# Kernel optimization log

Measured on AMD Instinct MI355X. Metric: run time of the kernel, lower is better.

Reference implementation:

```python
import jax, jax.numpy as jnp
import numpy as np

N, C, TX, TY = 32, 256, 1024, 1024


def setup_inputs() -> dict:
    key = jax.random.key(0)
    ks = jax.random.split(key, 9)
    s = 1.0 / np.sqrt(C)
    return {
        "Q": jax.random.normal(ks[0], (N, C, TY), dtype=jnp.float32),
        "K": jax.random.normal(ks[1], (N, C, TX), dtype=jnp.float32),
        "V": jax.random.normal(ks[2], (N, C, TX), dtype=jnp.float32),
        "Wq": jax.random.normal(ks[3], (C, C), dtype=jnp.float32) * s,
        "bq": jax.random.normal(ks[4], (C,), dtype=jnp.float32) * 0.01,
        "Wk": jax.random.normal(ks[5], (C, C), dtype=jnp.float32) * s,
        "bk": jax.random.normal(ks[6], (C,), dtype=jnp.float32) * 0.01,
        "Wv": jax.random.normal(ks[7], (C, C), dtype=jnp.float32) * s,
        "bv": jax.random.normal(ks[8], (C,), dtype=jnp.float32) * 0.01,
    }


def _proj_tanh(W, b, x):
    # 1x1 conv over channels: (C_out, C_in) x (N, C_in, T) -> (N, C_out, T)
    return jnp.tanh(jnp.einsum("oc,nct->not", W, x) + b[None, :, None])


def reference(Q, K, V, Wq, bq, Wk, bk, Wv, bv):
    d_k = Q.shape[1]
    Qp = _proj_tanh(Wq, bq, Q)  # (N, C, Ty)
    Kp = _proj_tanh(Wk, bk, K)  # (N, C, Tx)
    Vp = _proj_tanh(Wv, bv, V)  # (N, C, Tx)
    scores = jnp.einsum("ncs,nct->nst", Kp, Qp) / jnp.sqrt(
        jnp.asarray(d_k, dtype=Q.dtype)
    )  # (N, Tx, Ty)
    A = jax.nn.softmax(scores, axis=1)  # softmax over Tx (dim=1)
    R = jnp.einsum("ncs,nst->nct", Vp, A)  # (N, C, Ty)
    return (R, A)
```

## Files before the change

### kernel.cpp

```cpp
#include <hip/hip_runtime.h>
#include <stdint.h>

#define N_B 32
#define C_D 256
#define T_D 1024

typedef unsigned short u16;
typedef __attribute__((ext_vector_type(8))) short short8;
typedef __attribute__((ext_vector_type(4))) float f32x4;

__device__ __forceinline__ u16 f2bf(float f) {
    unsigned x = __float_as_uint(f);
    return (u16)((x + 0x7fffu + ((x >> 16) & 1u)) >> 16);
}

__device__ __forceinline__ void gld16(const void* g, void* l) {
    __builtin_amdgcn_global_load_lds(
        (const __attribute__((address_space(1))) uint32_t*)g,
        (__attribute__((address_space(3))) uint32_t*)l, 16, 0, 0);
}

__device__ __forceinline__ void comb(float& m, float& l, float m2, float l2) {
    float M = fmaxf(m, m2);
    l = l * __expf(m - M) + l2 * __expf(m2 - M);
    m = M;
}

__global__ __launch_bounds__(256) void conv_w(const float* __restrict__ w0,
                                              const float* __restrict__ w1,
                                              const float* __restrict__ w2,
                                              u16* __restrict__ o0,
                                              u16* __restrict__ o1,
                                              u16* __restrict__ o2) {
    const float* in = blockIdx.y == 0 ? w0 : (blockIdx.y == 1 ? w1 : w2);
    u16* out       = blockIdx.y == 0 ? o0 : (blockIdx.y == 1 ? o1 : o2);
    int i = blockIdx.x * 256 + threadIdx.x;
    out[i] = f2bf(in[i]);
}

template <bool NORM>
__device__ __forceinline__ void stage_tr(const float* src, u16* sm, int tid,
                                         const float* Mv, const float* Rv,
                                         float* adst, bool awr) {
    const int sr2 = tid >> 4;
    const int tt8 = (tid & 15) * 8;
    float4 v0 = *(const float4*)(src);
    float4 v1 = *(const float4*)(src + 4);
    float4 w0 = *(const float4*)(src + T_D);
    float4 w1 = *(const float4*)(src + T_D + 4);
    float a[8] = {v0.x, v0.y, v0.z, v0.w, v1.x, v1.y, v1.z, v1.w};
    float b[8] = {w0.x, w0.y, w0.z, w0.w, w1.x, w1.y, w1.z, w1.w};
    if constexpr (NORM) {
#pragma unroll
        for (int j = 0; j < 8; ++j) {
            a[j] = __expf(a[j] - Mv[j]) * Rv[j];
            b[j] = __expf(b[j] - Mv[j]) * Rv[j];
        }
        if (awr) {
            ((float4*)adst)[0]         = make_float4(a[0], a[1], a[2], a[3]);
            ((float4*)adst)[1]         = make_float4(a[4], a[5], a[6], a[7]);
            ((float4*)(adst + T_D))[0] = make_float4(b[0], b[1], b[2], b[3]);
            ((float4*)(adst + T_D))[1] = make_float4(b[4], b[5], b[6], b[7]);
        }
    }
    const int kk = sr2 * 2;
#pragma unroll
    for (int j = 0; j < 8; ++j) {
        const int t  = tt8 + j;
        const int ks = kk ^ (((t >> 4) & 3) << 3);
        uint32_t pk = (uint32_t)f2bf(a[j]) | ((uint32_t)f2bf(b[j]) << 16);
        *(uint32_t*)(sm + t * 32 + ks) = pk;
    }
}

template <bool TRA, bool TRB, int EPI, bool F32OUT>
__global__ __launch_bounds__(256) void gemm_t(
        const void* __restrict__ Av, const void* __restrict__ Bv,
        const float* __restrict__ bias, void* __restrict__ OutV,
        int Kdim, int ldo, long sA, long sB, long sO, float scale,
        float* __restrict__ Pm, float* __restrict__ Pl)
{
    __shared__ __align__(16) u16 smA[128 * 32];
    __shared__ __align__(16) u16 smB[128 * 32];

    const int nb = blockIdx.z;
    const int n0 = blockIdx.x * 128;
    const int m0 = blockIdx.y * 128;
    const int tid = threadIdx.x;

    const int srow = tid >> 2;
    const int sk8  = (tid & 3) * 8;
    const int sr2  = tid >> 4;
    const int tt8  = (tid & 15) * 8;

    const u16* gA0 = nullptr; const u16* gA1 = nullptr;
    const float* tA = nullptr;
    if constexpr (TRA) {
        tA = (const float*)Av + (size_t)nb * sA + (size_t)(sr2 * 2) * T_D + m0 + tt8;
    } else {
        const u16* Ab = (const u16*)Av + (size_t)nb * sA;
        gA0 = Ab + (size_t)(m0 + srow) * Kdim + sk8;
        gA1 = gA0 + (size_t)64 * Kdim;
    }
    const u16* gB0 = nullptr; const u16* gB1 = nullptr;
    const float* tB = nullptr;
    if constexpr (TRB) {
        tB = (const float*)Bv + (size_t)nb * sB + (size_t)(sr2 * 2) * T_D + n0 + tt8;
    } else {
        const u16* Bb = (const u16*)Bv + (size_t)nb * sB;
        gB0 = Bb + (size_t)(n0 + srow) * Kdim + sk8;
        gB1 = gB0 + (size_t)64 * Kdim;
    }
    u16* lA0 = smA + tid * 8; u16* lA1 = smA + 2048 + tid * 8;
    u16* lB0 = smB + tid * 8; u16* lB1 = smB + 2048 + tid * 8;

    const int lane = tid & 63;
    const int w    = tid >> 6;
    const int wm   = (w >> 1) * 64;
    const int wn   = (w & 1) * 64;
    const int l15  = lane & 15;
    const int quad = lane >> 4;

    f32x4 acc[4][4];
#pragma unroll
    for (int i = 0; i < 4; ++i)
#pragma unroll
        for (int j = 0; j < 4; ++j) acc[i][j] = (f32x4){0.f, 0.f, 0.f, 0.f};

    for (int kb = 0; kb < Kdim; kb += 32) {
        if constexpr (TRA) {
            stage_tr<false>(tA + (size_t)kb * T_D, smA, tid, nullptr, nullptr, nullptr, false);
        } else {
            gld16(gA0 + kb, lA0);
            gld16(gA1 + kb, lA1);
        }
        if constexpr (TRB) {
            stage_tr<false>(tB + (size_t)kb * T_D, smB, tid, nullptr, nullptr, nullptr, false);
        } else {
            gld16(gB0 + kb, lB0);
            gld16(gB1 + kb, lB1);
        }
        __syncthreads();
        short8 af[4], bfr[4];
#pragma unroll
        for (int i = 0; i < 4; ++i) {
            const int ra = wm + i * 16 + l15;
            const int ca = TRA ? ((quad ^ ((ra >> 4) & 3)) * 8) : (quad * 8);
            af[i] = *(const short8*)(smA + ra * 32 + ca);
            const int rb = wn + i * 16 + l15;
            const int cb = TRB ? ((quad ^ ((rb >> 4) & 3)) * 8) : (quad * 8);
            bfr[i] = *(const short8*)(smB + rb * 32 + cb);
        }
#pragma unroll
        for (int mi = 0; mi < 4; ++mi)
#pragma unroll
            for (int ni = 0; ni < 4; ++ni)
                acc[mi][ni] = __builtin_amdgcn_mfma_f32_16x16x32_bf16(
                        af[mi], bfr[ni], acc[mi][ni], 0, 0, 0);
        __syncthreads();
    }

    if constexpr (EPI == 3) {
        float pmv[4] = {-1e30f, -1e30f, -1e30f, -1e30f};
        float plv[4] = {0.f, 0.f, 0.f, 0.f};
#pragma unroll
        for (int mi = 0; mi < 4; ++mi) {
            const int mb = m0 + wm + mi * 16 + quad * 4;
#pragma unroll
            for (int r = 0; r < 4; ++r) {
                const int m = mb + r;
#pragma unroll
                for (int ni = 0; ni < 4; ++ni) {
                    const int nn = n0 + wn + ni * 16 + l15;
                    float v = acc[mi][ni][r] * scale;
                    ((float*)OutV)[(size_t)nb * sO + (size_t)m * ldo + nn] = v;
                    pmv[ni] = fmaxf(pmv[ni], v);
                }
            }
        }
#pragma unroll
        for (int ni = 0; ni < 4; ++ni) {
            float s = 0.f;
#pragma unroll
            for (int mi = 0; mi < 4; ++mi)
#pragma unroll
                for (int r = 0; r < 4; ++r)
                    s += __expf(acc[mi][ni][r] * scale - pmv[ni]);
            plv[ni] = s;
        }
#pragma unroll
        for (int ni = 0; ni < 4; ++ni) {
            float m = pmv[ni], l = plv[ni];
            float m2 = __shfl_xor(m, 16), l2 = __shfl_xor(l, 16);
            comb(m, l, m2, l2);
            m2 = __shfl_xor(m, 32); l2 = __shfl_xor(l, 32);
            comb(m, l, m2, l2);
            pmv[ni] = m; plv[ni] = l;
        }
        __shared__ float red_m[4][64];
        __shared__ float red_l[4][64];
        if (quad == 0) {
#pragma unroll
            for (int ni = 0; ni < 4; ++ni) {
                red_m[w][ni * 16 + l15] = pmv[ni];
                red_l[w][ni * 16 + l15] = plv[ni];
            }
        }
        __syncthreads();
        if (tid < 128) {
            const int half = tid >> 6, cc = tid & 63;
            float m = red_m[half][cc], l = red_l[half][cc];
            comb(m, l, red_m[half + 2][cc], red_l[half + 2][cc]);
            const size_t pi = ((size_t)nb * 8 + blockIdx.y) * T_D + n0 + tid;
            Pm[pi] = m; Pl[pi] = l;
        }
    } else {
#pragma unroll
        for (int mi = 0; mi < 4; ++mi) {
            const int mb = m0 + wm + mi * 16 + quad * 4;
#pragma unroll
            for (int r = 0; r < 4; ++r) {
                const int m = mb + r;
                float bm = 0.f;
                if (EPI == 2) bm = bias[m];
#pragma unroll
                for (int ni = 0; ni < 4; ++ni) {
                    const int nn = n0 + wn + ni * 16 + l15;
                    float v = acc[mi][ni][r] * scale;
                    if (EPI == 1) v = tanhf(v + bias[nn]);
                    if (EPI == 2) v = tanhf(v + bm);
                    if (F32OUT)
                        ((float*)OutV)[(size_t)nb * sO + (size_t)m * ldo + nn] = v;
                    else
                        ((u16*)OutV)[(size_t)nb * sO + (size_t)m * ldo + nn] = f2bf(v);
                }
            }
        }
    }
}

__global__ __launch_bounds__(256) void merge_ml(const float* __restrict__ Pm,
                                                const float* __restrict__ Pl,
                                                float* __restrict__ Mf,
                                                float* __restrict__ Rl) {
    const int i = blockIdx.x * 256 + threadIdx.x;
    const int n = i >> 10, t = i & (T_D - 1);
    const float* pm = Pm + (size_t)n * 8 * T_D + t;
    const float* pl = Pl + (size_t)n * 8 * T_D + t;
    float M = -1e30f;
#pragma unroll
    for (int j = 0; j < 8; ++j) M = fmaxf(M, pm[(size_t)j * T_D]);
    float L = 0.f;
#pragma unroll
    for (int j = 0; j < 8; ++j) L += pl[(size_t)j * T_D] * __expf(pm[(size_t)j * T_D] - M);
    Mf[i] = M;
    Rl[i] = 1.0f / L;
}

__global__ __launch_bounds__(512) void gemm_rn(
        const u16* __restrict__ Vp, float* S,
        const float* __restrict__ Mf, const float* __restrict__ Rl,
        float* __restrict__ R)
{
    __shared__ __align__(16) u16 smA[256 * 32];
    __shared__ __align__(16) u16 smB[128 * 32];

    const int nb  = blockIdx.z;
    const int n0  = blockIdx.x * 128;
    const int tid = threadIdx.x;

    const u16* Ab = Vp + (size_t)nb * (C_D * T_D);
    float* Sb = S + (size_t)nb * ((size_t)T_D * T_D);
    float* Rb = R + (size_t)nb * (C_D * T_D);

    const int srow = tid >> 2;
    const int sk8  = (tid & 3) * 8;
    const u16* gA0 = Ab + (size_t)srow * T_D + sk8;
    const u16* gA1 = gA0 + (size_t)128 * T_D;
    u16* lA0 = smA + tid * 8;
    u16* lA1 = smA + 4096 + tid * 8;

    float Mv[8], Rv[8];
    float* tB = nullptr;
    if (tid < 256) {
        const int sr2 = tid >> 4;
        const int tt8 = (tid & 15) * 8;
        tB = Sb + (size_t)(sr2 * 2) * T_D + n0 + tt8;
#pragma unroll
        for (int j = 0; j < 8; ++j) {
            Mv[j] = Mf[(size_t)nb * T_D + n0 + tt8 + j];
            Rv[j] = Rl[(size_t)nb * T_D + n0 + tt8 + j];
        }
    }

    const int lane = tid & 63;
    const int w    = tid >> 6;
    const int wm   = (w >> 1) * 64;
    const int wn   = (w & 1) * 64;
    const int l15  = lane & 15;
    const int quad = lane >> 4;

    f32x4 acc[4][4];
#pragma unroll
    for (int i = 0; i < 4; ++i)
#pragma unroll
        for (int j = 0; j < 4; ++j) acc[i][j] = (f32x4){0.f, 0.f, 0.f, 0.f};

    for (int kb = 0; kb < T_D; kb += 32) {
        gld16(gA0 + kb, lA0);
        gld16(gA1 + kb, lA1);
        if (tid < 256) {
            float* src = tB + (size_t)kb * T_D;
            stage_tr<true>(src, smB, tid, Mv, Rv, src, true);
        }
        __syncthreads();
        short8 af[4], bfr[4];
#pragma unroll
        for (int i = 0; i < 4; ++i) {
            af[i] = *(const short8*)(smA + (wm + i * 16 + l15) * 32 + quad * 8);
            const int rb = wn + i * 16 + l15;
            bfr[i] = *(const short8*)(smB + rb * 32 + ((quad ^ ((rb >> 4) & 3)) * 8));
        }
#pragma unroll
        for (int mi = 0; mi < 4; ++mi)
#pragma unroll
            for (int ni = 0; ni < 4; ++ni)
                acc[mi][ni] = __builtin_amdgcn_mfma_f32_16x16x32_bf16(
                        af[mi], bfr[ni], acc[mi][ni], 0, 0, 0);
        __syncthreads();
    }

#pragma unroll
    for (int mi = 0; mi < 4; ++mi) {
        const int mb = wm + mi * 16 + quad * 4;
#pragma unroll
        for (int r = 0; r < 4; ++r) {
            const int m = mb + r;
#pragma unroll
            for (int ni = 0; ni < 4; ++ni) {
                const int nn = n0 + wn + ni * 16 + l15;
                Rb[(size_t)m * T_D + nn] = acc[mi][ni][r];
            }
        }
    }
}

extern "C" void kernel_launch(void* const* d_in, const int* in_sizes, int n_in,
                              void* d_out, int out_size, void* d_ws, size_t ws_size,
                              hipStream_t stream) {
    const float* Qf = (const float*)d_in[0];
    const float* Kf = (const float*)d_in[1];
    const float* Vf = (const float*)d_in[2];
    const float* Wq = (const float*)d_in[3];
    const float* bq = (const float*)d_in[4];
    const float* Wk = (const float*)d_in[5];
    const float* bk = (const float*)d_in[6];
    const float* Wv = (const float*)d_in[7];
    const float* bv = (const float*)d_in[8];

    float* Rout = (float*)d_out;
    float* Aout = Rout + (size_t)N_B * C_D * T_D;

    u16* QpT = (u16*)Rout;
    u16* KpT = (u16*)Rout + 8388608;
    u16* Wqb = (u16*)Aout;
    u16* Wkb = Wqb + 65536;
    u16* Wvb = Wkb + 65536;
    u16* Vp  = (u16*)d_in[0];

    float* Pm = (float*)d_in[1];
    float* Pl = Pm + (size_t)N_B * 8 * T_D;
    float* Mf = Pl + (size_t)N_B * 8 * T_D;
    float* Rl = Mf + (size_t)N_B * T_D;

    dim3 blk(256);
    const long sX = (long)C_D * T_D;
    const long sS = (long)T_D * T_D;

    conv_w<<<dim3(256, 3), blk, 0, stream>>>(Wq, Wk, Wv, Wqb, Wkb, Wvb);

    gemm_t<true, false, 1, false><<<dim3(2, 8, N_B), blk, 0, stream>>>(
            Qf, Wqb, bq, QpT, C_D, C_D, sX, 0, sX, 1.0f, nullptr, nullptr);
    gemm_t<true, false, 1, false><<<dim3(2, 8, N_B), blk, 0, stream>>>(
            Kf, Wkb, bk, KpT, C_D, C_D, sX, 0, sX, 1.0f, nullptr, nullptr);
    gemm_t<false, true, 2, false><<<dim3(8, 2, N_B), blk, 0, stream>>>(
            Wvb, Vf, bv, Vp, C_D, T_D, 0, sX, sX, 1.0f, nullptr, nullptr);

    gemm_t<false, false, 3, true><<<dim3(8, 8, N_B), blk, 0, stream>>>(
            KpT, QpT, nullptr, Aout, C_D, T_D, sX, sX, sS, 0.0625f, Pm, Pl);

    merge_ml<<<dim3(128), blk, 0, stream>>>(Pm, Pl, Mf, Rl);

    gemm_rn<<<dim3(8, 1, N_B), dim3(512), 0, stream>>>(Vp, Aout, Mf, Rl, Rout);
}
```

Before: 389.7 us.

## Merge Q/K projection launches, swizzle LDS staging, halve gemm_rn tile width

Q and K projections now run in a single launch with a doubled grid z that selects pointers per block, removing one launch. The LDS layout for direct global_load_lds tiles gains an XOR swizzle on the k-chunk, applied both when staging and when reading, to reduce bank conflicts on MFMA operand reads. The final normalize-and-multiply GEMM uses 64-wide output tiles with twice as many blocks, raising occupancy across 256 CUs. The trade-off is that each block reuses V tiles less and the A matrix is read the same number of times in total.

New measurement: 381.3 us. 2.2% less time.

```diff
diff --git a/kernel.cpp b/kernel.cpp
--- a/kernel.cpp
+++ b/kernel.cpp
@@ -39,11 +39,10 @@
 }
 
 template <bool NORM>
-__device__ __forceinline__ void stage_tr(const float* src, u16* sm, int tid,
+__device__ __forceinline__ void stage_tr(const float* src, u16* sm,
+                                         int sr2, int tt8,
                                          const float* Mv, const float* Rv,
                                          float* adst, bool awr) {
-    const int sr2 = tid >> 4;
-    const int tt8 = (tid & 15) * 8;
     float4 v0 = *(const float4*)(src);
     float4 v1 = *(const float4*)(src + 4);
     float4 w0 = *(const float4*)(src + T_D);
@@ -73,23 +72,29 @@
     }
 }
 
-template <bool TRA, bool TRB, int EPI, bool F32OUT>
+template <bool TRA, bool TRB, int EPI, bool F32OUT, bool DUAL>
 __global__ __launch_bounds__(256) void gemm_t(
         const void* __restrict__ Av, const void* __restrict__ Bv,
         const float* __restrict__ bias, void* __restrict__ OutV,
         int Kdim, int ldo, long sA, long sB, long sO, float scale,
-        float* __restrict__ Pm, float* __restrict__ Pl)
+        float* __restrict__ Pm, float* __restrict__ Pl,
+        const void* __restrict__ Av2, const void* __restrict__ Bv2,
+        const float* __restrict__ bias2, void* __restrict__ Out2)
 {
     __shared__ __align__(16) u16 smA[128 * 32];
     __shared__ __align__(16) u16 smB[128 * 32];
 
-    const int nb = blockIdx.z;
+    int nb = blockIdx.z;
+    if (DUAL && nb >= N_B) {
+        nb -= N_B;
+        Av = Av2; Bv = Bv2; bias = bias2; OutV = Out2;
+    }
     const int n0 = blockIdx.x * 128;
     const int m0 = blockIdx.y * 128;
     const int tid = threadIdx.x;
 
     const int srow = tid >> 2;
-    const int sk8  = (tid & 3) * 8;
+    const int sk8  = (((tid & 3) ^ ((srow >> 1) & 3)) * 8);
     const int sr2  = tid >> 4;
     const int tt8  = (tid & 15) * 8;
 
@@ -129,13 +134,15 @@
 
     for (int kb = 0; kb < Kdim; kb += 32) {
         if constexpr (TRA) {
-            stage_tr<false>(tA + (size_t)kb * T_D, smA, tid, nullptr, nullptr, nullptr, false);
+            stage_tr<false>(tA + (size_t)kb * T_D, smA, sr2, tt8,
+                            nullptr, nullptr, nullptr, false);
         } else {
             gld16(gA0 + kb, lA0);
             gld16(gA1 + kb, lA1);
         }
         if constexpr (TRB) {
-            stage_tr<false>(tB + (size_t)kb * T_D, smB, tid, nullptr, nullptr, nullptr, false);
+            stage_tr<false>(tB + (size_t)kb * T_D, smB, sr2, tt8,
+                            nullptr, nullptr, nullptr, false);
         } else {
             gld16(gB0 + kb, lB0);
             gld16(gB1 + kb, lB1);
@@ -145,10 +152,12 @@
 #pragma unroll
         for (int i = 0; i < 4; ++i) {
             const int ra = wm + i * 16 + l15;
-            const int ca = TRA ? ((quad ^ ((ra >> 4) & 3)) * 8) : (quad * 8);
+            const int ca = TRA ? ((quad ^ ((ra >> 4) & 3)) * 8)
+                               : ((quad ^ ((ra >> 1) & 3)) * 8);
             af[i] = *(const short8*)(smA + ra * 32 + ca);
             const int rb = wn + i * 16 + l15;
-            const int cb = TRB ? ((quad ^ ((rb >> 4) & 3)) * 8) : (quad * 8);
+            const int cb = TRB ? ((quad ^ ((rb >> 4) & 3)) * 8)
+                               : ((quad ^ ((rb >> 1) & 3)) * 8);
             bfr[i] = *(const short8*)(smB + rb * 32 + cb);
         }
 #pragma unroll
@@ -263,10 +272,10 @@
         float* __restrict__ R)
 {
     __shared__ __align__(16) u16 smA[256 * 32];
-    __shared__ __align__(16) u16 smB[128 * 32];
+    __shared__ __align__(16) u16 smB[64 * 32];
 
     const int nb  = blockIdx.z;
-    const int n0  = blockIdx.x * 128;
+    const int n0  = blockIdx.x * 64;
     const int tid = threadIdx.x;
 
     const u16* Ab = Vp + (size_t)nb * (C_D * T_D);
@@ -274,7 +283,7 @@
     float* Rb = R + (size_t)nb * (C_D * T_D);
 
     const int srow = tid >> 2;
-    const int sk8  = (tid & 3) * 8;
+    const int sk8  = (((tid & 3) ^ ((srow >> 1) & 3)) * 8);
     const u16* gA0 = Ab + (size_t)srow * T_D + sk8;
     const u16* gA1 = gA0 + (size_t)128 * T_D;
     u16* lA0 = smA + tid * 8;
@@ -282,49 +291,54 @@
 
     float Mv[8], Rv[8];
     float* tB = nullptr;
-    if (tid < 256) {
-        const int sr2 = tid >> 4;
-        const int tt8 = (tid & 15) * 8;
-        tB = Sb + (size_t)(sr2 * 2) * T_D + n0 + tt8;
+    int bsr2 = 0, btt8 = 0;
+    if (tid < 128) {
+        bsr2 = tid >> 3;
+        btt8 = (tid & 7) * 8;
+        tB = Sb + (size_t)(bsr2 * 2) * T_D + n0 + btt8;
 #pragma unroll
         for (int j = 0; j < 8; ++j) {
-            Mv[j] = Mf[(size_t)nb * T_D + n0 + tt8 + j];
-            Rv[j] = Rl[(size_t)nb * T_D + n0 + tt8 + j];
+            Mv[j] = Mf[(size_t)nb * T_D + n0 + btt8 + j];
+            Rv[j] = Rl[(size_t)nb * T_D + n0 + btt8 + j];
         }
     }
 
     const int lane = tid & 63;
     const int w    = tid >> 6;
     const int wm   = (w >> 1) * 64;
-    const int wn   = (w & 1) * 64;
+    const int wn   = (w & 1) * 32;
     const int l15  = lane & 15;
     const int quad = lane >> 4;
 
-    f32x4 acc[4][4];
+    f32x4 acc[4][2];
 #pragma unroll
     for (int i = 0; i < 4; ++i)
 #pragma unroll
-        for (int j = 0; j < 4; ++j) acc[i][j] = (f32x4){0.f, 0.f, 0.f, 0.f};
+        for (int j = 0; j < 2; ++j) acc[i][j] = (f32x4){0.f, 0.f, 0.f, 0.f};
 
     for (int kb = 0; kb < T_D; kb += 32) {
         gld16(gA0 + kb, lA0);
         gld16(gA1 + kb, lA1);
-        if (tid < 256) {
+        if (tid < 128) {
             float* src = tB + (size_t)kb * T_D;
-            stage_tr<true>(src, smB, tid, Mv, Rv, src, true);
+            stage_tr<true>(src, smB, bsr2, btt8, Mv, Rv, src, true);
         }
         __syncthreads();
-        short8 af[4], bfr[4];
+        short8 af[4], bfr[2];
 #pragma unroll
         for (int i = 0; i < 4; ++i) {
-            af[i] = *(const short8*)(smA + (wm + i * 16 + l15) * 32 + quad * 8);
+            const int ra = wm + i * 16 + l15;
+            af[i] = *(const short8*)(smA + ra * 32 + ((quad ^ ((ra >> 1) & 3)) * 8));
+        }
+#pragma unroll
+        for (int i = 0; i < 2; ++i) {
             const int rb = wn + i * 16 + l15;
             bfr[i] = *(const short8*)(smB + rb * 32 + ((quad ^ ((rb >> 4) & 3)) * 8));
         }
 #pragma unroll
         for (int mi = 0; mi < 4; ++mi)
 #pragma unroll
-            for (int ni = 0; ni < 4; ++ni)
+            for (int ni = 0; ni < 2; ++ni)
                 acc[mi][ni] = __builtin_amdgcn_mfma_f32_16x16x32_bf16(
                         af[mi], bfr[ni], acc[mi][ni], 0, 0, 0);
         __syncthreads();
@@ -337,7 +351,7 @@
         for (int r = 0; r < 4; ++r) {
             const int m = mb + r;
 #pragma unroll
-            for (int ni = 0; ni < 4; ++ni) {
+            for (int ni = 0; ni < 2; ++ni) {
                 const int nn = n0 + wn + ni * 16 + l15;
                 Rb[(size_t)m * T_D + nn] = acc[mi][ni][r];
             }
@@ -379,17 +393,18 @@
 
     conv_w<<<dim3(256, 3), blk, 0, stream>>>(Wq, Wk, Wv, Wqb, Wkb, Wvb);
 
-    gemm_t<true, false, 1, false><<<dim3(2, 8, N_B), blk, 0, stream>>>(
-            Qf, Wqb, bq, QpT, C_D, C_D, sX, 0, sX, 1.0f, nullptr, nullptr);
-    gemm_t<true, false, 1, false><<<dim3(2, 8, N_B), blk, 0, stream>>>(
-            Kf, Wkb, bk, KpT, C_D, C_D, sX, 0, sX, 1.0f, nullptr, nullptr);
-    gemm_t<false, true, 2, false><<<dim3(8, 2, N_B), blk, 0, stream>>>(
-            Wvb, Vf, bv, Vp, C_D, T_D, 0, sX, sX, 1.0f, nullptr, nullptr);
-
-    gemm_t<false, false, 3, true><<<dim3(8, 8, N_B), blk, 0, stream>>>(
-            KpT, QpT, nullptr, Aout, C_D, T_D, sX, sX, sS, 0.0625f, Pm, Pl);
+    gemm_t<true, false, 1, false, true><<<dim3(2, 8, 2 * N_B), blk, 0, stream>>>(
+            Qf, Wqb, bq, QpT, C_D, C_D, sX, 0, sX, 1.0f, nullptr, nullptr,
+            Kf, Wkb, bk, KpT);
+    gemm_t<false, true, 2, false, false><<<dim3(8, 2, N_B), blk, 0, stream>>>(
+            Wvb, Vf, bv, Vp, C_D, T_D, 0, sX, sX, 1.0f, nullptr, nullptr,
+            nullptr, nullptr, nullptr, nullptr);
+
+    gemm_t<false, false, 3, true, false><<<dim3(8, 8, N_B), blk, 0, stream>>>(
+            KpT, QpT, nullptr, Aout, C_D, T_D, sX, sX, sS, 0.0625f, Pm, Pl,
+            nullptr, nullptr, nullptr, nullptr);
 
     merge_ml<<<dim3(128), blk, 0, stream>>>(Pm, Pl, Mf, Rl);
 
-    gemm_rn<<<dim3(8, 1, N_B), dim3(512), 0, stream>>>(Vp, Aout, Mf, Rl, Rout);
-}
+    gemm_rn<<<dim3(16, 1, N_B), dim3(512), 0, stream>>>(Vp, Aout, Mf, Rl, Rout);
+}
```
